# Kernel optimization log

Hardware: AMD Instinct MI355X
Metric: run time of the kernel (lower is better)

The kernel has to match this reference:

```python
import jax, jax.numpy as jnp
import numpy as np

N_NODES = 100000
N_EDGES = 1600000
C_IN = 64
C_OUT = 128
EPS = 1e-5


def _layer_norm(x, gamma, beta):
    # node-wise LayerNorm over feature dim
    mu = jnp.mean(x, axis=-1, keepdims=True)
    var = jnp.mean(jnp.square(x - mu), axis=-1, keepdims=True)
    return (x - mu) * jax.lax.rsqrt(var + EPS) * gamma + beta


def _graph_conv(x, src, dst, w_root, w_nbr, b):
    # GraphConv: out_i = x_i @ w_root + (sum_{j in N(i)} x_j) @ w_nbr + b
    # aggregate-then-transform (valid since message is linear) to save memory
    agg = jax.ops.segment_sum(x[src], dst, num_segments=N_NODES)
    return x @ w_root + agg @ w_nbr + b


def setup_inputs() -> dict:
    key = jax.random.key(0)
    ks = jax.random.split(key, 10)
    s_in = 1.0 / np.sqrt(C_IN)
    s_out = 1.0 / np.sqrt(C_OUT)
    x = jax.random.normal(ks[0], (N_NODES, C_IN), dtype=jnp.float32)
    edge_index = jax.random.randint(ks[1], (2, N_EDGES), 0, N_NODES, dtype=jnp.int32)
    return {
        "x": x,
        "edge_index": edge_index,
        "w_root0": jax.random.normal(ks[2], (C_IN, C_OUT), jnp.float32) * s_in,
        "w_nbr0": jax.random.normal(ks[3], (C_IN, C_OUT), jnp.float32) * s_in,
        "b0": jnp.zeros((C_OUT,), jnp.float32),
        "w_root1": jax.random.normal(ks[4], (C_OUT, C_OUT), jnp.float32) * s_out,
        "w_nbr1": jax.random.normal(ks[5], (C_OUT, C_OUT), jnp.float32) * s_out,
        "b1": jnp.zeros((C_OUT,), jnp.float32),
        "gamma0": jnp.ones((C_OUT,), jnp.float32),
        "beta0": jnp.zeros((C_OUT,), jnp.float32),
        "gamma1": jnp.ones((C_OUT,), jnp.float32),
        "beta1": jnp.zeros((C_OUT,), jnp.float32),
        "w_lin": jax.random.normal(ks[6], (C_IN, C_OUT), jnp.float32) * s_in,
        "b_lin": jnp.zeros((C_OUT,), jnp.float32),
    }


def reference(x, edge_index, w_root0, w_nbr0, b0, w_root1, w_nbr1, b1,
              gamma0, beta0, gamma1, beta1, w_lin, b_lin):
    src, dst = edge_index[0], edge_index[1]
    y = _graph_conv(x, src, dst, w_root0, w_nbr0, b0)
    y = jax.nn.relu(_layer_norm(y, gamma0, beta0))
    y = _graph_conv(y, src, dst, w_root1, w_nbr1, b1)
    out = y + (x @ w_lin + b_lin)  # Conv1d(k=1) residual projection
    out = jax.nn.relu(_layer_norm(out, gamma1, beta1))
    return out
```

## Files before the change

### kernel.cpp

```cpp
#include <hip/hip_runtime.h>

#define CIN 64
#define COUT 128
#define BSH 9
#define NB2 196
#define BCAP 10240
#define CURPAD 16
#define EPB 8192
constexpr float LN_EPS = 1e-5f;

typedef __attribute__((ext_vector_type(8))) short    bf16x8;
typedef __attribute__((ext_vector_type(4))) float    f32x4;
typedef __attribute__((ext_vector_type(8))) unsigned short us8;

__device__ inline float b2f(unsigned short u) {
    union { unsigned int i; float f; } v; v.i = ((unsigned int)u) << 16; return v.f;
}
__device__ inline unsigned short f2b(float f) {
    union { float f; unsigned int i; } v; v.f = f;
    unsigned int x = v.i;
    return (unsigned short)((x + 0x7FFFu + ((x >> 16) & 1u)) >> 16);
}

__global__ __launch_bounds__(256) void fused_prep(
    const int* __restrict__ src, const int* __restrict__ dst,
    const float* __restrict__ x,
    const float* __restrict__ wr0, const float* __restrict__ wn0,
    const float* __restrict__ wr1, const float* __restrict__ wn1,
    const float* __restrict__ wl,
    int* __restrict__ bcur, unsigned int* __restrict__ bstage,
    unsigned short* __restrict__ ab0, unsigned short* __restrict__ a1,
    unsigned short* __restrict__ wp0, unsigned short* __restrict__ wp1,
    int n_nodes, int n_edges, int eblk, int cblk)
{
    __shared__ unsigned int  ent[EPB];
    __shared__ unsigned char ebk[EPB];
    __shared__ int cnt[NB2], gb[NB2], lcur[NB2];

    const int bid = blockIdx.x;
    const int t = threadIdx.x;
    if (bid < eblk) {
        const int e0 = bid * EPB;
        const int n = min(EPB, n_edges - e0);
        for (int i = t; i < NB2; i += 256) cnt[i] = 0;
        __syncthreads();
        for (int i = t; i < n; i += 256) {
            const int d = dst[e0 + i];
            ent[i] = ((unsigned int)(d & 511) << 17) | (unsigned int)src[e0 + i];
            const int b = d >> BSH;
            ebk[i] = (unsigned char)b;
            atomicAdd(&cnt[b], 1);
        }
        __syncthreads();
        for (int i = t; i < NB2; i += 256) {
            gb[i] = (cnt[i] > 0) ? atomicAdd(&bcur[i * CURPAD], cnt[i]) : 0;
            lcur[i] = 0;
        }
        __syncthreads();
        for (int i = t; i < n; i += 256) {
            const int b = ebk[i];
            const int pos = gb[b] + atomicAdd(&lcur[b], 1);
            if (pos < BCAP) bstage[(size_t)b * BCAP + pos] = ent[i];
        }
    } else if (bid < eblk + cblk) {
        int tt = (bid - eblk) * 256 + t;
        int node = tt >> 4;
        if (node >= n_nodes) return;
        int c = (tt & 15) << 2;
        const float4 v = *reinterpret_cast<const float4*>(x + (size_t)node * CIN + c);
        unsigned int lo = (unsigned int)f2b(v.x) | ((unsigned int)f2b(v.y) << 16);
        unsigned int hi = (unsigned int)f2b(v.z) | ((unsigned int)f2b(v.w) << 16);
        unsigned int* p0 = (unsigned int*)(ab0 + (size_t)node * 128 + c);
        p0[0] = lo; p0[1] = hi;
        unsigned int* p1 = (unsigned int*)(a1 + (size_t)node * 320 + 256 + c);
        p1[0] = lo; p1[1] = hi;
    } else {
        int tt = (bid - eblk - cblk) * 256 + t;
        if (tt < 8 * 4 * 64 * 8) {
            const int j = tt & 7, idx = tt >> 3;
            const int lane = idx & 63, fk = idx >> 6;
            const int nt = fk >> 2, ks = fk & 3;
            const int n = nt * 16 + (lane & 15);
            const int k = ks * 32 + (lane >> 4) * 8 + j;
            const float v = (k < 64) ? wr0[k * COUT + n] : wn0[(k - 64) * COUT + n];
            wp0[tt] = f2b(v);
        } else {
            const int t2 = tt - 8 * 4 * 64 * 8;
            if (t2 >= 8 * 10 * 64 * 8) return;
            const int j = t2 & 7, idx = t2 >> 3;
            const int lane = idx & 63, fk = idx >> 6;
            const int nt = fk / 10, ks = fk % 10;
            const int n = nt * 16 + (lane & 15);
            const int k = ks * 32 + (lane >> 4) * 8 + j;
            float v;
            if (k < 128)      v = wr1[k * COUT + n];
            else if (k < 256) v = wn1[(k - 128) * COUT + n];
            else              v = wl[(k - 256) * COUT + n];
            wp1[t2] = f2b(v);
        }
    }
}

__global__ __launch_bounds__(256) void bucket_csr(
    unsigned int* __restrict__ bstage,
    const int* __restrict__ bcur,
    int* __restrict__ rowptr, int* __restrict__ deg, int n_nodes)
{
    __shared__ unsigned int ent[BCAP];
    __shared__ int cnt[512], base[512], lc[512];
    __shared__ int sc[2][512];

    const int b = blockIdx.x;
    const int t = threadIdx.x;
    const int nb = min(bcur[b * CURPAD], BCAP);
    unsigned int* bk = bstage + (size_t)b * BCAP;

    for (int i = t; i < 512; i += 256) cnt[i] = 0;
    __syncthreads();
    for (int i = t; i < nb; i += 256) {
        const unsigned int p = bk[i];
        ent[i] = p;
        atomicAdd(&cnt[p >> 17], 1);
    }
    __syncthreads();
    for (int i = t; i < 512; i += 256) sc[0][i] = cnt[i];
    __syncthreads();
    int pin = 0;
#pragma unroll
    for (int off = 1; off < 512; off <<= 1) {
        for (int i = t; i < 512; i += 256) {
            int v = sc[pin][i];
            if (i >= off) v += sc[pin][i - off];
            sc[pin ^ 1][i] = v;
        }
        __syncthreads();
        pin ^= 1;
    }
    for (int i = t; i < 512; i += 256) {
        const int bs = sc[pin][i] - cnt[i];
        base[i] = bs; lc[i] = 0;
        const int d = (b << BSH) + i;
        if (d < n_nodes) { rowptr[d] = b * BCAP + bs; deg[d] = cnt[i]; }
    }
    __syncthreads();
    __shared__ unsigned int sorted[BCAP];
    for (int i = t; i < nb; i += 256) {
        const unsigned int p = ent[i];
        const int dl = p >> 17;
        const int pos = base[dl] + atomicAdd(&lc[dl], 1);
        sorted[pos] = p & 0x1FFFFu;
    }
    __syncthreads();
    for (int i = t; i < nb; i += 256) bk[i] = sorted[i];
}


__global__ __launch_bounds__(256) void gather_c64(
    unsigned short* __restrict__ ab0, const int* __restrict__ rowptr,
    const int* __restrict__ deg, const unsigned int* __restrict__ es, int n_nodes)
{
    const int node = blockIdx.x * 16 + (threadIdx.x >> 4);
    if (node >= n_nodes) return;
    const int lane = threadIdx.x & 63;
    const int fr = lane & 15;
    const int gbase = lane & 48;
    const int start = rowptr[node];
    const int len = deg[node];
    float a0 = 0.f, a1v = 0.f, a2 = 0.f, a3 = 0.f;

    for (int k0 = 0; k0 < len; k0 += 16) {
        const int m = min(16, len - k0);
        const int my = (fr < m) ? (int)es[start + k0 + fr] : 0;
        int j = 0;
        for (; j + 1 < m; j += 2) {
            const int s0 = __shfl(my, gbase + j);
            const int s1 = __shfl(my, gbase + j + 1);
            const unsigned long long u0 =
                *(const unsigned long long*)(ab0 + (size_t)s0 * 128 + fr * 4);
            const unsigned long long u1 =
                *(const unsigned long long*)(ab0 + (size_t)s1 * 128 + fr * 4);
            a0  += b2f((unsigned short)u0) + b2f((unsigned short)u1);
            a1v += b2f((unsigned short)(u0 >> 16)) + b2f((unsigned short)(u1 >> 16));
            a2  += b2f((unsigned short)(u0 >> 32)) + b2f((unsigned short)(u1 >> 32));
            a3  += b2f((unsigned short)(u0 >> 48)) + b2f((unsigned short)(u1 >> 48));
        }
        if (j < m) {
            const int s0 = __shfl(my, gbase + j);
            const unsigned long long u0 =
                *(const unsigned long long*)(ab0 + (size_t)s0 * 128 + fr * 4);
            a0  += b2f((unsigned short)u0);
            a1v += b2f((unsigned short)(u0 >> 16));
            a2  += b2f((unsigned short)(u0 >> 32));
            a3  += b2f((unsigned short)(u0 >> 48));
        }
    }
    const unsigned long long p = (unsigned long long)f2b(a0)
        | ((unsigned long long)f2b(a1v) << 16)
        | ((unsigned long long)f2b(a2)  << 32)
        | ((unsigned long long)f2b(a3)  << 48);
    *(unsigned long long*)(ab0 + (size_t)node * 128 + 64 + fr * 4) = p;
}

__global__ __launch_bounds__(256) void gather_c128(
    unsigned short* __restrict__ a1, const int* __restrict__ rowptr,
    const int* __restrict__ deg, const unsigned int* __restrict__ es, int n_nodes)
{
    const int node = blockIdx.x * 16 + (threadIdx.x >> 4);
    if (node >= n_nodes) return;
    const int lane = threadIdx.x & 63;
    const int fr = lane & 15;
    const int gbase = lane & 48;
    const int start = rowptr[node];
    const int len = deg[node];
    float acc[8] = {0.f, 0.f, 0.f, 0.f, 0.f, 0.f, 0.f, 0.f};

    for (int k0 = 0; k0 < len; k0 += 16) {
        const int m = min(16, len - k0);
        const int my = (fr < m) ? (int)es[start + k0 + fr] : 0;
        int j = 0;
        for (; j + 1 < m; j += 2) {
            const int s0 = __shfl(my, gbase + j);
            const int s1 = __shfl(my, gbase + j + 1);
            const us8 r0 = *(const us8*)(a1 + (size_t)s0 * 320 + fr * 8);
            const us8 r1 = *(const us8*)(a1 + (size_t)s1 * 320 + fr * 8);
#pragma unroll
            for (int q = 0; q < 8; q++) acc[q] += b2f(r0[q]) + b2f(r1[q]);
        }
        if (j < m) {
            const int s0 = __shfl(my, gbase + j);
            const us8 r0 = *(const us8*)(a1 + (size_t)s0 * 320 + fr * 8);
#pragma unroll
            for (int q = 0; q < 8; q++) acc[q] += b2f(r0[q]);
        }
    }
    us8 p;
#pragma unroll
    for (int q = 0; q < 8; q++) p[q] = f2b(acc[q]);
    *(us8*)(a1 + (size_t)node * 320 + 128 + fr * 8) = p;
}


__global__ __launch_bounds__(256) void conv0_mfma(
    const unsigned short* __restrict__ A,
    const unsigned short* __restrict__ Wpk,
    const float* __restrict__ b, const float* __restrict__ gamma,
    const float* __restrict__ beta,
    unsigned short* __restrict__ Yout,
    int n_nodes)
{
    __shared__ unsigned short lt[4][16 * 136];
    const int wid = threadIdx.x >> 6;
    const int lane = threadIdx.x & 63;
    const int m0 = blockIdx.x * 64 + wid * 16;
    if (m0 >= n_nodes) return;
    const int g = lane >> 4, fr = lane & 15;

    const bf16x8* Ap = reinterpret_cast<const bf16x8*>(A + (size_t)(m0 + fr) * 128) + g;
    bf16x8 a[4];
#pragma unroll
    for (int ks = 0; ks < 4; ks++) a[ks] = Ap[ks * 4];

    f32x4 acc[8];
    float gm[8], bt[8];
#pragma unroll
    for (int nt = 0; nt < 8; nt++) {
        const int col = nt * 16 + fr;
        const float bb = b[col];
        acc[nt] = (f32x4){bb, bb, bb, bb};
        gm[nt] = gamma[col]; bt[nt] = beta[col];
    }

    const bf16x8* Wp = reinterpret_cast<const bf16x8*>(Wpk) + lane;
#pragma unroll
    for (int nt = 0; nt < 8; nt++) {
        bf16x8 w[4];
#pragma unroll
        for (int ks = 0; ks < 4; ks++) w[ks] = Wp[(nt * 4 + ks) * 64];
#pragma unroll
        for (int ks = 0; ks < 4; ks++)
            acc[nt] = __builtin_amdgcn_mfma_f32_16x16x32_bf16(a[ks], w[ks], acc[nt], 0, 0, 0);
    }

#pragma unroll
    for (int r = 0; r < 4; r++) {
        float s = 0.f, s2 = 0.f;
#pragma unroll
        for (int nt = 0; nt < 8; nt++) { const float v = acc[nt][r]; s += v; s2 += v * v; }
#pragma unroll
        for (int off = 1; off < 16; off <<= 1) {
            s += __shfl_xor(s, off); s2 += __shfl_xor(s2, off);
        }
        const float mu = s * (1.0f / COUT);
        const float var = s2 * (1.0f / COUT) - mu * mu;
        const float rstd = rsqrtf(var + LN_EPS);
        const int lrow = g * 4 + r;
#pragma unroll
        for (int nt = 0; nt < 8; nt++) {
            const float v = fmaxf((acc[nt][r] - mu) * rstd * gm[nt] + bt[nt], 0.0f);
            lt[wid][lrow * 136 + nt * 16 + fr] = f2b(v);
        }
    }

#pragma unroll
    for (int i = 0; i < 4; i++) {
        const int chunk = i * 64 + lane;
        const int row = chunk >> 4, seg = chunk & 15;
        if (m0 + row < n_nodes) {
            us8 v = *reinterpret_cast<const us8*>(&lt[wid][row * 136 + seg * 8]);
            *reinterpret_cast<us8*>(Yout + (size_t)(m0 + row) * 320 + seg * 8) = v;
        }
    }
}

__global__ __launch_bounds__(256) void conv1_mfma(
    const unsigned short* __restrict__ A,
    const unsigned short* __restrict__ Wpk,
    const float* __restrict__ b1, const float* __restrict__ bl,
    const float* __restrict__ gamma, const float* __restrict__ beta,
    float* __restrict__ Out, int n_nodes)
{
    __shared__ float lt[4][16 * 132];
    const int wid = threadIdx.x >> 6;
    const int lane = threadIdx.x & 63;
    const int m0 = blockIdx.x * 64 + wid * 16;
    if (m0 >= n_nodes) return;
    const int g = lane >> 4, fr = lane & 15;

    const bf16x8* Ap = reinterpret_cast<const bf16x8*>(A + (size_t)(m0 + fr) * 320) + g;
    bf16x8 a[10];
#pragma unroll
    for (int ks = 0; ks < 10; ks++) a[ks] = Ap[ks * 4];

    f32x4 acc[8];
    float gm[8], bt[8];
#pragma unroll
    for (int nt = 0; nt < 8; nt++) {
        const int col = nt * 16 + fr;
        const float bb = b1[col] + bl[col];
        acc[nt] = (f32x4){bb, bb, bb, bb};
        gm[nt] = gamma[col]; bt[nt] = beta[col];
    }

    const bf16x8* Wp = reinterpret_cast<const bf16x8*>(Wpk) + lane;
#pragma unroll
    for (int nt = 0; nt < 8; nt++) {
        bf16x8 w[10];
#pragma unroll
        for (int ks = 0; ks < 10; ks++) w[ks] = Wp[(nt * 10 + ks) * 64];
#pragma unroll
        for (int ks = 0; ks < 10; ks++)
            acc[nt] = __builtin_amdgcn_mfma_f32_16x16x32_bf16(a[ks], w[ks], acc[nt], 0, 0, 0);
    }

#pragma unroll
    for (int r = 0; r < 4; r++) {
        float s = 0.f, s2 = 0.f;
#pragma unroll
        for (int nt = 0; nt < 8; nt++) { const float v = acc[nt][r]; s += v; s2 += v * v; }
#pragma unroll
        for (int off = 1; off < 16; off <<= 1) {
            s += __shfl_xor(s, off); s2 += __shfl_xor(s2, off);
        }
        const float mu = s * (1.0f / COUT);
        const float var = s2 * (1.0f / COUT) - mu * mu;
        const float rstd = rsqrtf(var + LN_EPS);
        const int lrow = g * 4 + r;
#pragma unroll
        for (int nt = 0; nt < 8; nt++) {
            const float v = fmaxf((acc[nt][r] - mu) * rstd * gm[nt] + bt[nt], 0.0f);
            lt[wid][lrow * 132 + nt * 16 + fr] = v;
        }
    }

#pragma unroll
    for (int i = 0; i < 8; i++) {
        const int chunk = i * 64 + lane;
        const int row = chunk >> 5, seg = chunk & 31;
        if (m0 + row < n_nodes) {
            f32x4 v = *reinterpret_cast<const f32x4*>(&lt[wid][row * 132 + seg * 4]);
            __builtin_nontemporal_store(
                v, reinterpret_cast<f32x4*>(Out + (size_t)(m0 + row) * 128 + seg * 4));
        }
    }
}

extern "C" void kernel_launch(void* const* d_in, const int* in_sizes, int n_in,
                              void* d_out, int out_size, void* d_ws, size_t ws_size,
                              hipStream_t stream)
{
    const float* x       = (const float*)d_in[0];
    const int*   ei      = (const int*)d_in[1];
    const float* w_root0 = (const float*)d_in[2];
    const float* w_nbr0  = (const float*)d_in[3];
    const float* b0      = (const float*)d_in[4];
    const float* w_root1 = (const float*)d_in[5];
    const float* w_nbr1  = (const float*)d_in[6];
    const float* b1      = (const float*)d_in[7];
    const float* gamma0  = (const float*)d_in[8];
    const float* beta0   = (const float*)d_in[9];
    const float* gamma1  = (const float*)d_in[10];
    const float* beta1   = (const float*)d_in[11];
    const float* w_lin   = (const float*)d_in[12];
    const float* b_lin   = (const float*)d_in[13];
    float* out = (float*)d_out;

    const int n_nodes = in_sizes[0] / CIN;
    const int n_edges = in_sizes[1] / 2;
    const int* src = ei;
    const int* dst = ei + n_edges;
    const int npad = (n_nodes + 63) & ~63;
    const int nbuck = (n_nodes + (1 << BSH) - 1) >> BSH;

    char* ws = (char*)d_ws;
    unsigned short* ab0 = (unsigned short*)ws;
    unsigned short* a1  = ab0 + (size_t)npad * 128;
    unsigned short* wp0 = a1 + (size_t)npad * 320;
    unsigned short* wp1 = wp0 + 8 * 4 * 64 * 8;
    int*  bcur   = (int*)(wp1 + 8 * 10 * 64 * 8);
    int*  rowptr = bcur + (size_t)nbuck * CURPAD;
    int*  deg    = rowptr + n_nodes;
    unsigned int* bstage = (unsigned int*)(deg + n_nodes);

    const int eblk = (n_edges + EPB - 1) / EPB;
    const int cblk = (n_nodes * 16 + 255) / 256;
    const int wblk = (8 * 4 * 64 * 8 + 8 * 10 * 64 * 8 + 255) / 256;
    const int nblk64 = npad / 64;
    const int nblk16 = (n_nodes + 15) / 16;

    hipMemsetAsync(bcur, 0, (size_t)nbuck * CURPAD * sizeof(int), stream);
    fused_prep<<<eblk + cblk + wblk, 256, 0, stream>>>(
        src, dst, x, w_root0, w_nbr0, w_root1, w_nbr1, w_lin,
        bcur, bstage, ab0, a1, wp0, wp1, n_nodes, n_edges, eblk, cblk);
    bucket_csr<<<nbuck, 256, 0, stream>>>(bstage, bcur, rowptr, deg, n_nodes);

    gather_c64<<<nblk16, 256, 0, stream>>>(ab0, rowptr, deg, bstage, n_nodes);
    conv0_mfma<<<nblk64, 256, 0, stream>>>(ab0, wp0, b0, gamma0, beta0, a1, n_nodes);

    gather_c128<<<nblk16, 256, 0, stream>>>(a1, rowptr, deg, bstage, n_nodes);
    conv1_mfma<<<nblk64, 256, 0, stream>>>(a1, wp1, b1, b_lin, gamma1, beta1, out, n_nodes);
}
```

Baseline: 193.5 us.

## Shrink layer-1 activation buffer, reuse bf16 x, widen c64 gather loads

Measured after the change: 202.7 us. 1.05x slower.

```diff
diff --git a/kernel.cpp b/kernel.cpp
--- a/kernel.cpp
+++ b/kernel.cpp
@@ -29,7 +29,7 @@
     const float* __restrict__ wr1, const float* __restrict__ wn1,
     const float* __restrict__ wl,
     int* __restrict__ bcur, unsigned int* __restrict__ bstage,
-    unsigned short* __restrict__ ab0, unsigned short* __restrict__ a1,
+    unsigned short* __restrict__ ab0,
     unsigned short* __restrict__ wp0, unsigned short* __restrict__ wp1,
     int n_nodes, int n_edges, int eblk, int cblk)
 {
@@ -72,8 +72,6 @@
         unsigned int hi = (unsigned int)f2b(v.z) | ((unsigned int)f2b(v.w) << 16);
         unsigned int* p0 = (unsigned int*)(ab0 + (size_t)node * 128 + c);
         p0[0] = lo; p0[1] = hi;
-        unsigned int* p1 = (unsigned int*)(a1 + (size_t)node * 320 + 256 + c);
-        p1[0] = lo; p1[1] = hi;
     } else {
         int tt = (bid - eblk - cblk) * 256 + t;
         if (tt < 8 * 4 * 64 * 8) {
@@ -143,20 +141,55 @@
         if (d < n_nodes) { rowptr[d] = b * BCAP + bs; deg[d] = cnt[i]; }
     }
     __syncthreads();
-    __shared__ unsigned int sorted[BCAP];
     for (int i = t; i < nb; i += 256) {
         const unsigned int p = ent[i];
         const int dl = p >> 17;
         const int pos = base[dl] + atomicAdd(&lc[dl], 1);
-        sorted[pos] = p & 0x1FFFFu;
-    }
-    __syncthreads();
-    for (int i = t; i < nb; i += 256) bk[i] = sorted[i];
+        bk[pos] = p & 0x1FFFFu;
+    }
 }
 
 
 __global__ __launch_bounds__(256) void gather_c64(
     unsigned short* __restrict__ ab0, const int* __restrict__ rowptr,
+    const int* __restrict__ deg, const unsigned int* __restrict__ es, int n_nodes)
+{
+    const int node = blockIdx.x * 32 + (threadIdx.x >> 3);
+    if (node >= n_nodes) return;
+    const int lane = threadIdx.x & 63;
+    const int fr = lane & 7;
+    const int gbase = lane & 56;
+    const int start = __builtin_nontemporal_load(rowptr + node);
+    const int len = __builtin_nontemporal_load(deg + node);
+    float acc[8] = {0.f, 0.f, 0.f, 0.f, 0.f, 0.f, 0.f, 0.f};
+
+    for (int k0 = 0; k0 < len; k0 += 8) {
+        const int m = min(8, len - k0);
+        const int my = (fr < m) ? (int)__builtin_nontemporal_load(es + start + k0 + fr) : 0;
+        int j = 0;
+        for (; j + 1 < m; j += 2) {
+            const int s0 = __shfl(my, gbase + j);
+            const int s1 = __shfl(my, gbase + j + 1);
+            const us8 r0 = *(const us8*)(ab0 + (size_t)s0 * 128 + fr * 8);
+            const us8 r1 = *(const us8*)(ab0 + (size_t)s1 * 128 + fr * 8);
+#pragma unroll
+            for (int q = 0; q < 8; q++) acc[q] += b2f(r0[q]) + b2f(r1[q]);
+        }
+        if (j < m) {
+            const int s0 = __shfl(my, gbase + j);
+            const us8 r0 = *(const us8*)(ab0 + (size_t)s0 * 128 + fr * 8);
+#pragma unroll
+            for (int q = 0; q < 8; q++) acc[q] += b2f(r0[q]);
+        }
+    }
+    us8 p;
+#pragma unroll
+    for (int q = 0; q < 8; q++) p[q] = f2b(acc[q]);
+    __builtin_nontemporal_store(p, (us8*)(ab0 + (size_t)node * 128 + 64 + fr * 8));
+}
+
+__global__ __launch_bounds__(256) void gather_c128(
+    unsigned short* __restrict__ a1, const int* __restrict__ rowptr,
     const int* __restrict__ deg, const unsigned int* __restrict__ es, int n_nodes)
 {
     const int node = blockIdx.x * 16 + (threadIdx.x >> 4);
@@ -164,71 +197,25 @@
     const int lane = threadIdx.x & 63;
     const int fr = lane & 15;
     const int gbase = lane & 48;
-    const int start = rowptr[node];
-    const int len = deg[node];
-    float a0 = 0.f, a1v = 0.f, a2 = 0.f, a3 = 0.f;
+    const int start = __builtin_nontemporal_load(rowptr + node);
+    const int len = __builtin_nontemporal_load(deg + node);
+    float acc[8] = {0.f, 0.f, 0.f, 0.f, 0.f, 0.f, 0.f, 0.f};
 
     for (int k0 = 0; k0 < len; k0 += 16) {
         const int m = min(16, len - k0);
-        const int my = (fr < m) ? (int)es[start + k0 + fr] : 0;
+        const int my = (fr < m) ? (int)__builtin_nontemporal_load(es + start + k0 + fr) : 0;
         int j = 0;
         for (; j + 1 < m; j += 2) {
             const int s0 = __shfl(my, gbase + j);
             const int s1 = __shfl(my, gbase + j + 1);
-            const unsigned long long u0 =
-                *(const unsigned long long*)(ab0 + (size_t)s0 * 128 + fr * 4);
-            const unsigned long long u1 =
-                *(const unsigned long long*)(ab0 + (size_t)s1 * 128 + fr * 4);
-            a0  += b2f((unsigned short)u0) + b2f((unsigned short)u1);
-            a1v += b2f((unsigned short)(u0 >> 16)) + b2f((unsigned short)(u1 >> 16));
-            a2  += b2f((unsigned short)(u0 >> 32)) + b2f((unsigned short)(u1 >> 32));
-            a3  += b2f((unsigned short)(u0 >> 48)) + b2f((unsigned short)(u1 >> 48));
+            const us8 r0 = *(const us8*)(a1 + (size_t)s0 * 256 + fr * 8);
+            const us8 r1 = *(const us8*)(a1 + (size_t)s1 * 256 + fr * 8);
+#pragma unroll
+            for (int q = 0; q < 8; q++) acc[q] += b2f(r0[q]) + b2f(r1[q]);
         }
         if (j < m) {
             const int s0 = __shfl(my, gbase + j);
-            const unsigned long long u0 =
-                *(const unsigned long long*)(ab0 + (size_t)s0 * 128 + fr * 4);
-            a0  += b2f((unsigned short)u0);
-            a1v += b2f((unsigned short)(u0 >> 16));
-            a2  += b2f((unsigned short)(u0 >> 32));
-            a3  += b2f((unsigned short)(u0 >> 48));
-        }
-    }
-    const unsigned long long p = (unsigned long long)f2b(a0)
-        | ((unsigned long long)f2b(a1v) << 16)
-        | ((unsigned long long)f2b(a2)  << 32)
-        | ((unsigned long long)f2b(a3)  << 48);
-    *(unsigned long long*)(ab0 + (size_t)node * 128 + 64 + fr * 4) = p;
-}
-
-__global__ __launch_bounds__(256) void gather_c128(
-    unsigned short* __restrict__ a1, const int* __restrict__ rowptr,
-    const int* __restrict__ deg, const unsigned int* __restrict__ es, int n_nodes)
-{
-    const int node = blockIdx.x * 16 + (threadIdx.x >> 4);
-    if (node >= n_nodes) return;
-    const int lane = threadIdx.x & 63;
-    const int fr = lane & 15;
-    const int gbase = lane & 48;
-    const int start = rowptr[node];
-    const int len = deg[node];
-    float acc[8] = {0.f, 0.f, 0.f, 0.f, 0.f, 0.f, 0.f, 0.f};
-
-    for (int k0 = 0; k0 < len; k0 += 16) {
-        const int m = min(16, len - k0);
-        const int my = (fr < m) ? (int)es[start + k0 + fr] : 0;
-        int j = 0;
-        for (; j + 1 < m; j += 2) {
-            const int s0 = __shfl(my, gbase + j);
-            const int s1 = __shfl(my, gbase + j + 1);
-            const us8 r0 = *(const us8*)(a1 + (size_t)s0 * 320 + fr * 8);
-            const us8 r1 = *(const us8*)(a1 + (size_t)s1 * 320 + fr * 8);
-#pragma unroll
-            for (int q = 0; q < 8; q++) acc[q] += b2f(r0[q]) + b2f(r1[q]);
-        }
-        if (j < m) {
-            const int s0 = __shfl(my, gbase + j);
-            const us8 r0 = *(const us8*)(a1 + (size_t)s0 * 320 + fr * 8);
+            const us8 r0 = *(const us8*)(a1 + (size_t)s0 * 256 + fr * 8);
 #pragma unroll
             for (int q = 0; q < 8; q++) acc[q] += b2f(r0[q]);
         }
@@ -236,7 +223,7 @@
     us8 p;
 #pragma unroll
     for (int q = 0; q < 8; q++) p[q] = f2b(acc[q]);
-    *(us8*)(a1 + (size_t)node * 320 + 128 + fr * 8) = p;
+    __builtin_nontemporal_store(p, (us8*)(a1 + (size_t)node * 256 + 128 + fr * 8));
 }
 
 
@@ -307,13 +294,14 @@
         const int row = chunk >> 4, seg = chunk & 15;
         if (m0 + row < n_nodes) {
             us8 v = *reinterpret_cast<const us8*>(&lt[wid][row * 136 + seg * 8]);
-            *reinterpret_cast<us8*>(Yout + (size_t)(m0 + row) * 320 + seg * 8) = v;
+            *reinterpret_cast<us8*>(Yout + (size_t)(m0 + row) * 256 + seg * 8) = v;
         }
     }
 }
 
 __global__ __launch_bounds__(256) void conv1_mfma(
-    const unsigned short* __restrict__ A,
+    const unsigned short* __restrict__ A1,
+    const unsigned short* __restrict__ A0,
     const unsigned short* __restrict__ Wpk,
     const float* __restrict__ b1, const float* __restrict__ bl,
     const float* __restrict__ gamma, const float* __restrict__ beta,
@@ -326,10 +314,13 @@
     if (m0 >= n_nodes) return;
     const int g = lane >> 4, fr = lane & 15;
 
-    const bf16x8* Ap = reinterpret_cast<const bf16x8*>(A + (size_t)(m0 + fr) * 320) + g;
+    const bf16x8* Ap1 = reinterpret_cast<const bf16x8*>(A1 + (size_t)(m0 + fr) * 256) + g;
+    const bf16x8* Ap0 = reinterpret_cast<const bf16x8*>(A0 + (size_t)(m0 + fr) * 128) + g;
     bf16x8 a[10];
 #pragma unroll
-    for (int ks = 0; ks < 10; ks++) a[ks] = Ap[ks * 4];
+    for (int ks = 0; ks < 8; ks++) a[ks] = Ap1[ks * 4];
+    a[8] = Ap0[0];
+    a[9] = Ap0[4];
 
     f32x4 acc[8];
     float gm[8], bt[8];
@@ -414,7 +405,7 @@
     char* ws = (char*)d_ws;
     unsigned short* ab0 = (unsigned short*)ws;
     unsigned short* a1  = ab0 + (size_t)npad * 128;
-    unsigned short* wp0 = a1 + (size_t)npad * 320;
+    unsigned short* wp0 = a1 + (size_t)npad * 256;
     unsigned short* wp1 = wp0 + 8 * 4 * 64 * 8;
     int*  bcur   = (int*)(wp1 + 8 * 10 * 64 * 8);
     int*  rowptr = bcur + (size_t)nbuck * CURPAD;
@@ -426,16 +417,17 @@
     const int wblk = (8 * 4 * 64 * 8 + 8 * 10 * 64 * 8 + 255) / 256;
     const int nblk64 = npad / 64;
     const int nblk16 = (n_nodes + 15) / 16;
+    const int nblk32 = (n_nodes + 31) / 32;
 
     hipMemsetAsync(bcur, 0, (size_t)nbuck * CURPAD * sizeof(int), stream);
     fused_prep<<<eblk + cblk + wblk, 256, 0, stream>>>(
         src, dst, x, w_root0, w_nbr0, w_root1, w_nbr1, w_lin,
-        bcur, bstage, ab0, a1, wp0, wp1, n_nodes, n_edges, eblk, cblk);
+        bcur, bstage, ab0, wp0, wp1, n_nodes, n_edges, eblk, cblk);
     bucket_csr<<<nbuck, 256, 0, stream>>>(bstage, bcur, rowptr, deg, n_nodes);
 
-    gather_c64<<<nblk16, 256, 0, stream>>>(ab0, rowptr, deg, bstage, n_nodes);
+    gather_c64<<<nblk32, 256, 0, stream>>>(ab0, rowptr, deg, bstage, n_nodes);
     conv0_mfma<<<nblk64, 256, 0, stream>>>(ab0, wp0, b0, gamma0, beta0, a1, n_nodes);
 
     gather_c128<<<nblk16, 256, 0, stream>>>(a1, rowptr, deg, bstage, n_nodes);
-    conv1_mfma<<<nblk64, 256, 0, stream>>>(a1, wp1, b1, b_lin, gamma1, beta1, out, n_nodes);
-}
+    conv1_mfma<<<nblk64, 256, 0, stream>>>(a1, ab0, wp1, b1, b_lin, gamma1, beta1, out, n_nodes);
+}
```

## Fuse neighbor gather into MFMA conv kernels and compact activation buffers

Applied to the files above, without the earlier changes.

Result: slower. 204.3 us (+5.6%).

```diff
diff --git a/kernel.cpp b/kernel.cpp
--- a/kernel.cpp
+++ b/kernel.cpp
@@ -29,7 +29,7 @@
     const float* __restrict__ wr1, const float* __restrict__ wn1,
     const float* __restrict__ wl,
     int* __restrict__ bcur, unsigned int* __restrict__ bstage,
-    unsigned short* __restrict__ ab0, unsigned short* __restrict__ a1,
+    unsigned short* __restrict__ ab0,
     unsigned short* __restrict__ wp0, unsigned short* __restrict__ wp1,
     int n_nodes, int n_edges, int eblk, int cblk)
 {
@@ -70,10 +70,8 @@
         const float4 v = *reinterpret_cast<const float4*>(x + (size_t)node * CIN + c);
         unsigned int lo = (unsigned int)f2b(v.x) | ((unsigned int)f2b(v.y) << 16);
         unsigned int hi = (unsigned int)f2b(v.z) | ((unsigned int)f2b(v.w) << 16);
-        unsigned int* p0 = (unsigned int*)(ab0 + (size_t)node * 128 + c);
+        unsigned int* p0 = (unsigned int*)(ab0 + (size_t)node * 64 + c);
         p0[0] = lo; p0[1] = hi;
-        unsigned int* p1 = (unsigned int*)(a1 + (size_t)node * 320 + 256 + c);
-        p1[0] = lo; p1[1] = hi;
     } else {
         int tt = (bid - eblk - cblk) * 256 + t;
         if (tt < 8 * 4 * 64 * 8) {
@@ -154,111 +152,79 @@
     for (int i = t; i < nb; i += 256) bk[i] = sorted[i];
 }
 
-
-__global__ __launch_bounds__(256) void gather_c64(
-    unsigned short* __restrict__ ab0, const int* __restrict__ rowptr,
-    const int* __restrict__ deg, const unsigned int* __restrict__ es, int n_nodes)
-{
-    const int node = blockIdx.x * 16 + (threadIdx.x >> 4);
-    if (node >= n_nodes) return;
-    const int lane = threadIdx.x & 63;
-    const int fr = lane & 15;
-    const int gbase = lane & 48;
-    const int start = rowptr[node];
-    const int len = deg[node];
-    float a0 = 0.f, a1v = 0.f, a2 = 0.f, a3 = 0.f;
-
-    for (int k0 = 0; k0 < len; k0 += 16) {
-        const int m = min(16, len - k0);
-        const int my = (fr < m) ? (int)es[start + k0 + fr] : 0;
-        int j = 0;
-        for (; j + 1 < m; j += 2) {
-            const int s0 = __shfl(my, gbase + j);
-            const int s1 = __shfl(my, gbase + j + 1);
-            const unsigned long long u0 =
-                *(const unsigned long long*)(ab0 + (size_t)s0 * 128 + fr * 4);
-            const unsigned long long u1 =
-                *(const unsigned long long*)(ab0 + (size_t)s1 * 128 + fr * 4);
-            a0  += b2f((unsigned short)u0) + b2f((unsigned short)u1);
-            a1v += b2f((unsigned short)(u0 >> 16)) + b2f((unsigned short)(u1 >> 16));
-            a2  += b2f((unsigned short)(u0 >> 32)) + b2f((unsigned short)(u1 >> 32));
-            a3  += b2f((unsigned short)(u0 >> 48)) + b2f((unsigned short)(u1 >> 48));
-        }
-        if (j < m) {
-            const int s0 = __shfl(my, gbase + j);
-            const unsigned long long u0 =
-                *(const unsigned long long*)(ab0 + (size_t)s0 * 128 + fr * 4);
-            a0  += b2f((unsigned short)u0);
-            a1v += b2f((unsigned short)(u0 >> 16));
-            a2  += b2f((unsigned short)(u0 >> 32));
-            a3  += b2f((unsigned short)(u0 >> 48));
-        }
-    }
-    const unsigned long long p = (unsigned long long)f2b(a0)
-        | ((unsigned long long)f2b(a1v) << 16)
-        | ((unsigned long long)f2b(a2)  << 32)
-        | ((unsigned long long)f2b(a3)  << 48);
-    *(unsigned long long*)(ab0 + (size_t)node * 128 + 64 + fr * 4) = p;
-}
-
-__global__ __launch_bounds__(256) void gather_c128(
-    unsigned short* __restrict__ a1, const int* __restrict__ rowptr,
-    const int* __restrict__ deg, const unsigned int* __restrict__ es, int n_nodes)
-{
-    const int node = blockIdx.x * 16 + (threadIdx.x >> 4);
-    if (node >= n_nodes) return;
-    const int lane = threadIdx.x & 63;
-    const int fr = lane & 15;
-    const int gbase = lane & 48;
-    const int start = rowptr[node];
-    const int len = deg[node];
-    float acc[8] = {0.f, 0.f, 0.f, 0.f, 0.f, 0.f, 0.f, 0.f};
-
-    for (int k0 = 0; k0 < len; k0 += 16) {
-        const int m = min(16, len - k0);
-        const int my = (fr < m) ? (int)es[start + k0 + fr] : 0;
-        int j = 0;
-        for (; j + 1 < m; j += 2) {
-            const int s0 = __shfl(my, gbase + j);
-            const int s1 = __shfl(my, gbase + j + 1);
-            const us8 r0 = *(const us8*)(a1 + (size_t)s0 * 320 + fr * 8);
-            const us8 r1 = *(const us8*)(a1 + (size_t)s1 * 320 + fr * 8);
-#pragma unroll
-            for (int q = 0; q < 8; q++) acc[q] += b2f(r0[q]) + b2f(r1[q]);
-        }
-        if (j < m) {
-            const int s0 = __shfl(my, gbase + j);
-            const us8 r0 = *(const us8*)(a1 + (size_t)s0 * 320 + fr * 8);
-#pragma unroll
-            for (int q = 0; q < 8; q++) acc[q] += b2f(r0[q]);
-        }
-    }
-    us8 p;
-#pragma unroll
-    for (int q = 0; q < 8; q++) p[q] = f2b(acc[q]);
-    *(us8*)(a1 + (size_t)node * 320 + 128 + fr * 8) = p;
-}
-
-
-__global__ __launch_bounds__(256) void conv0_mfma(
-    const unsigned short* __restrict__ A,
+__global__ __launch_bounds__(256) void fused_conv0(
+    const unsigned short* __restrict__ X,
+    const int* __restrict__ rowptr, const int* __restrict__ deg,
+    const unsigned int* __restrict__ es,
     const unsigned short* __restrict__ Wpk,
     const float* __restrict__ b, const float* __restrict__ gamma,
     const float* __restrict__ beta,
     unsigned short* __restrict__ Yout,
     int n_nodes)
 {
+    __shared__ unsigned short agg[64][72];
     __shared__ unsigned short lt[4][16 * 136];
-    const int wid = threadIdx.x >> 6;
-    const int lane = threadIdx.x & 63;
-    const int m0 = blockIdx.x * 64 + wid * 16;
-    if (m0 >= n_nodes) return;
+
+    const int tid = threadIdx.x;
+    const int lane = tid & 63;
+    const int node0 = blockIdx.x * 64;
+
+    {
+        const int fr = lane & 15;
+        const int gbase = lane & 48;
+#pragma unroll
+        for (int p = 0; p < 4; p++) {
+            const int nl = p * 16 + (tid >> 4);
+            const int node = node0 + nl;
+            const bool ok = (node < n_nodes);
+            const int start = ok ? rowptr[node] : 0;
+            const int len = ok ? deg[node] : 0;
+            float a0 = 0.f, a1v = 0.f, a2 = 0.f, a3 = 0.f;
+            for (int k0 = 0; k0 < len; k0 += 16) {
+                const int m = min(16, len - k0);
+                const int my = (fr < m) ? (int)es[start + k0 + fr] : 0;
+                int j = 0;
+                for (; j + 1 < m; j += 2) {
+                    const int s0 = __shfl(my, gbase + j);
+                    const int s1 = __shfl(my, gbase + j + 1);
+                    const unsigned long long u0 =
+                        *(const unsigned long long*)(X + (size_t)s0 * 64 + fr * 4);
+                    const unsigned long long u1 =
+                        *(const unsigned long long*)(X + (size_t)s1 * 64 + fr * 4);
+                    a0  += b2f((unsigned short)u0) + b2f((unsigned short)u1);
+                    a1v += b2f((unsigned short)(u0 >> 16)) + b2f((unsigned short)(u1 >> 16));
+                    a2  += b2f((unsigned short)(u0 >> 32)) + b2f((unsigned short)(u1 >> 32));
+                    a3  += b2f((unsigned short)(u0 >> 48)) + b2f((unsigned short)(u1 >> 48));
+                }
+                if (j < m) {
+                    const int s0 = __shfl(my, gbase + j);
+                    const unsigned long long u0 =
+                        *(const unsigned long long*)(X + (size_t)s0 * 64 + fr * 4);
+                    a0  += b2f((unsigned short)u0);
+                    a1v += b2f((unsigned short)(u0 >> 16));
+                    a2  += b2f((unsigned short)(u0 >> 32));
+                    a3  += b2f((unsigned short)(u0 >> 48));
+                }
+            }
+            const unsigned long long pk = (unsigned long long)f2b(a0)
+                | ((unsigned long long)f2b(a1v) << 16)
+                | ((unsigned long long)f2b(a2)  << 32)
+                | ((unsigned long long)f2b(a3)  << 48);
+            *(unsigned long long*)(&agg[nl][fr * 4]) = pk;
+        }
+    }
+    __syncthreads();
+
+    const int wid = tid >> 6;
+    const int m0 = node0 + wid * 16;
     const int g = lane >> 4, fr = lane & 15;
 
-    const bf16x8* Ap = reinterpret_cast<const bf16x8*>(A + (size_t)(m0 + fr) * 128) + g;
+    const bf16x8* Xp = reinterpret_cast<const bf16x8*>(X + (size_t)(m0 + fr) * 64) + g;
     bf16x8 a[4];
-#pragma unroll
-    for (int ks = 0; ks < 4; ks++) a[ks] = Ap[ks * 4];
+    a[0] = Xp[0];
+    a[1] = Xp[4];
+    a[2] = *reinterpret_cast<const bf16x8*>(&agg[wid * 16 + fr][g * 8]);
+    a[3] = *reinterpret_cast<const bf16x8*>(&agg[wid * 16 + fr][32 + g * 8]);
 
     f32x4 acc[8];
     float gm[8], bt[8];
@@ -307,29 +273,82 @@
         const int row = chunk >> 4, seg = chunk & 15;
         if (m0 + row < n_nodes) {
             us8 v = *reinterpret_cast<const us8*>(&lt[wid][row * 136 + seg * 8]);
-            *reinterpret_cast<us8*>(Yout + (size_t)(m0 + row) * 320 + seg * 8) = v;
-        }
-    }
-}
-
-__global__ __launch_bounds__(256) void conv1_mfma(
-    const unsigned short* __restrict__ A,
+            *reinterpret_cast<us8*>(Yout + (size_t)(m0 + row) * 128 + seg * 8) = v;
+        }
+    }
+}
+
+__global__ __launch_bounds__(256) void fused_conv1(
+    const unsigned short* __restrict__ Y,
+    const unsigned short* __restrict__ X,
+    const int* __restrict__ rowptr, const int* __restrict__ deg,
+    const unsigned int* __restrict__ es,
     const unsigned short* __restrict__ Wpk,
     const float* __restrict__ b1, const float* __restrict__ bl,
     const float* __restrict__ gamma, const float* __restrict__ beta,
     float* __restrict__ Out, int n_nodes)
 {
-    __shared__ float lt[4][16 * 132];
-    const int wid = threadIdx.x >> 6;
-    const int lane = threadIdx.x & 63;
-    const int m0 = blockIdx.x * 64 + wid * 16;
-    if (m0 >= n_nodes) return;
+    __shared__ __align__(16) char smem[33792];
+    unsigned short (*agg)[136] = reinterpret_cast<unsigned short(*)[136]>(smem);
+    float* lt = reinterpret_cast<float*>(smem);
+
+    const int tid = threadIdx.x;
+    const int lane = tid & 63;
+    const int node0 = blockIdx.x * 64;
+
+    {
+        const int fr = lane & 15;
+        const int gbase = lane & 48;
+#pragma unroll
+        for (int p = 0; p < 4; p++) {
+            const int nl = p * 16 + (tid >> 4);
+            const int node = node0 + nl;
+            const bool ok = (node < n_nodes);
+            const int start = ok ? rowptr[node] : 0;
+            const int len = ok ? deg[node] : 0;
+            float acc[8] = {0.f, 0.f, 0.f, 0.f, 0.f, 0.f, 0.f, 0.f};
+            for (int k0 = 0; k0 < len; k0 += 16) {
+                const int m = min(16, len - k0);
+                const int my = (fr < m) ? (int)es[start + k0 + fr] : 0;
+                int j = 0;
+                for (; j + 1 < m; j += 2) {
+                    const int s0 = __shfl(my, gbase + j);
+                    const int s1 = __shfl(my, gbase + j + 1);
+                    const us8 r0 = *(const us8*)(Y + (size_t)s0 * 128 + fr * 8);
+                    const us8 r1 = *(const us8*)(Y + (size_t)s1 * 128 + fr * 8);
+#pragma unroll
+                    for (int q = 0; q < 8; q++) acc[q] += b2f(r0[q]) + b2f(r1[q]);
+                }
+                if (j < m) {
+                    const int s0 = __shfl(my, gbase + j);
+                    const us8 r0 = *(const us8*)(Y + (size_t)s0 * 128 + fr * 8);
+#pragma unroll
+                    for (int q = 0; q < 8; q++) acc[q] += b2f(r0[q]);
+                }
+            }
+            us8 pk;
+#pragma unroll
+            for (int q = 0; q < 8; q++) pk[q] = f2b(acc[q]);
+            *reinterpret_cast<us8*>(&agg[nl][fr * 8]) = pk;
+        }
+    }
+    __syncthreads();
+
+    const int wid = tid >> 6;
+    const int m0 = node0 + wid * 16;
     const int g = lane >> 4, fr = lane & 15;
 
-    const bf16x8* Ap = reinterpret_cast<const bf16x8*>(A + (size_t)(m0 + fr) * 320) + g;
+    const bf16x8* Yp = reinterpret_cast<const bf16x8*>(Y + (size_t)(m0 + fr) * 128) + g;
+    const bf16x8* Xp = reinterpret_cast<const bf16x8*>(X + (size_t)(m0 + fr) * 64) + g;
     bf16x8 a[10];
 #pragma unroll
-    for (int ks = 0; ks < 10; ks++) a[ks] = Ap[ks * 4];
+    for (int ks = 0; ks < 4; ks++) a[ks] = Yp[ks * 4];
+#pragma unroll
+    for (int ks = 0; ks < 4; ks++)
+        a[4 + ks] = *reinterpret_cast<const bf16x8*>(&agg[wid * 16 + fr][ks * 32 + g * 8]);
+    a[8] = Xp[0];
+    a[9] = Xp[4];
+    __syncthreads();
 
     f32x4 acc[8];
     float gm[8], bt[8];
@@ -368,7 +387,7 @@
 #pragma unroll
         for (int nt = 0; nt < 8; nt++) {
             const float v = fmaxf((acc[nt][r] - mu) * rstd * gm[nt] + bt[nt], 0.0f);
-            lt[wid][lrow * 132 + nt * 16 + fr] = v;
+            lt[wid * (16 * 132) + lrow * 132 + nt * 16 + fr] = v;
         }
     }
 
@@ -377,7 +396,7 @@
         const int chunk = i * 64 + lane;
         const int row = chunk >> 5, seg = chunk & 31;
         if (m0 + row < n_nodes) {
-            f32x4 v = *reinterpret_cast<const f32x4*>(&lt[wid][row * 132 + seg * 4]);
+            f32x4 v = *reinterpret_cast<const f32x4*>(&lt[wid * (16 * 132) + row * 132 + seg * 4]);
             __builtin_nontemporal_store(
                 v, reinterpret_cast<f32x4*>(Out + (size_t)(m0 + row) * 128 + seg * 4));
         }
@@ -413,8 +432,8 @@
 
     char* ws = (char*)d_ws;
     unsigned short* ab0 = (unsigned short*)ws;
-    unsigned short* a1  = ab0 + (size_t)npad * 128;
-    unsigned short* wp0 = a1 + (size_t)npad * 320;
+    unsigned short* a1  = ab0 + (size_t)npad * 64;
+    unsigned short* wp0 = a1 + (size_t)npad * 128;
     unsigned short* wp1 = wp0 + 8 * 4 * 64 * 8;
     int*  bcur   = (int*)(wp1 + 8 * 10 * 64 * 8);
     int*  rowptr = bcur + (size_t)nbuck * CURPAD;
@@ -425,17 +444,16 @@
     const int cblk = (n_nodes * 16 + 255) / 256;
     const int wblk = (8 * 4 * 64 * 8 + 8 * 10 * 64 * 8 + 255) / 256;
     const int nblk64 = npad / 64;
-    const int nblk16 = (n_nodes + 15) / 16;
 
     hipMemsetAsync(bcur, 0, (size_t)nbuck * CURPAD * sizeof(int), stream);
     fused_prep<<<eblk + cblk + wblk, 256, 0, stream>>>(
         src, dst, x, w_root0, w_nbr0, w_root1, w_nbr1, w_lin,
-        bcur, bstage, ab0, a1, wp0, wp1, n_nodes, n_edges, eblk, cblk);
+        bcur, bstage, ab0, wp0, wp1, n_nodes, n_edges, eblk, cblk);
     bucket_csr<<<nbuck, 256, 0, stream>>>(bstage, bcur, rowptr, deg, n_nodes);
 
-    gather_c64<<<nblk16, 256, 0, stream>>>(ab0, rowptr, deg, bstage, n_nodes);
-    conv0_mfma<<<nblk64, 256, 0, stream>>>(ab0, wp0, b0, gamma0, beta0, a1, n_nodes);
-
-    gather_c128<<<nblk16, 256, 0, stream>>>(a1, rowptr, deg, bstage, n_nodes);
-    conv1_mfma<<<nblk64, 256, 0, stream>>>(a1, wp1, b1, b_lin, gamma1, beta1, out, n_nodes);
-}
+    fused_conv0<<<nblk64, 256, 0, stream>>>(ab0, rowptr, deg, bstage, wp0,
+                                            b0, gamma0, beta0, a1, n_nodes);
+
+    fused_conv1<<<nblk64, 256, 0, stream>>>(a1, ab0, rowptr, deg, bstage, wp1,
+                                            b1, b_lin, gamma1, beta1, out, n_nodes);
+}
```
